# Optimization experiments

Measured on AMD Instinct MI355X. Metric: run time of the kernel, lower is better.

Reference implementation:

```python
import jax, jax.numpy as jnp
import numpy as np

N_BITS = 4            # W4A4 duquant-style fake quantization
BLOCK = 128           # rotation block size


def _round_ste(x):
    # straight-through rounding (matches round_ste used by LLM quantizers)
    return x + jax.lax.stop_gradient(jnp.round(x) - x)


def _block_rotate(x, R):
    # apply block-diagonal rotation along the last dim: x[..., F] -> x[..., F]
    *lead, F = x.shape
    B = R.shape[0]
    xr = jnp.einsum('...kb,bc->...kc', x.reshape(*lead, F // B, B), R)
    return xr.reshape(*lead, F)


def _fake_quant(x, R, n_bits):
    # rotate -> dynamic asymmetric uniform quant over last dim -> dequant -> de-rotate
    qmax = 2 ** n_bits - 1
    xr = _block_rotate(x, R)
    xmin = jnp.minimum(xr.min(axis=-1, keepdims=True), 0.0)
    xmax = jnp.maximum(xr.max(axis=-1, keepdims=True), 0.0)
    scale = jnp.clip((xmax - xmin) / qmax, 1e-5, None)
    zero_point = jax.lax.stop_gradient(jnp.round(-xmin / scale))
    xq = jnp.clip(_round_ste(xr / scale) + zero_point, 0.0, float(qmax))
    xdq = (xq - zero_point) * scale
    return _block_rotate(xdq, R.T)


def setup_inputs() -> dict:
    key = jax.random.key(0)
    k1, k2, k3 = jax.random.split(key, 3)
    x = jax.random.normal(k1, (4, 2048, 4096), dtype=jnp.float32)
    weight = jax.random.normal(k2, (4096, 4096), dtype=jnp.float32) * 0.02
    bias = jax.random.normal(k3, (4096,), dtype=jnp.float32) * 0.01
    # fixed orthogonal rotation matrix (DuQuant learned/constructed rotation)
    rng = np.random.default_rng(0)
    Rnp, _ = np.linalg.qr(rng.standard_normal((BLOCK, BLOCK)).astype(np.float32))
    R = jnp.asarray(Rnp, dtype=jnp.float32)
    return {"input": x, "weight": weight, "bias": bias, "R": R}


def reference(input, weight, bias, R):
    # act fake-quant (use_act_quant=True), weight fake-quant (use_weight_quant=True)
    x_q = _fake_quant(input, R, N_BITS)        # [B, S, Fin]
    w_q = _fake_quant(weight, R, N_BITS)       # [Fout, Fin], per-out-channel quant
    out = jnp.einsum('bsi,oi->bso', x_q, w_q) + bias
    return out
```

## Files before the change

kernel.cpp:

```cpp
#include <hip/hip_runtime.h>
#include <hip/hip_bf16.h>
#include <stdint.h>


typedef __bf16    bf16x8 __attribute__((ext_vector_type(8)));
typedef float     f32x4  __attribute__((ext_vector_type(4)));
typedef int       i32x4  __attribute__((ext_vector_type(4)));
typedef uint32_t  u32;
typedef uint32_t  u32x4  __attribute__((ext_vector_type(4)));

__device__ __forceinline__ void gload_lds16(const void* g, void* l) {
  __builtin_amdgcn_global_load_lds(
      (__attribute__((address_space(1))) void*)(g),
      (__attribute__((address_space(3))) void*)(l), 16, 0, 0);
}

__global__ __launch_bounds__(256)
void prep_rt(const float* __restrict__ R, unsigned short* __restrict__ RT3)
{
  const int tid = blockIdx.x * 256 + threadIdx.x;
  const int q  = tid & 7;
  const int l  = (tid >> 3) & 63;
  const int f  = (tid >> 9) & 7;
  const int ks = tid >> 12;
  const float v = R[(ks * 32 + (l >> 4) * 8 + q) * 128 + f * 16 + (l & 15)];
  __hip_bfloat16 h1 = __float2bfloat16(v);
  const float rem = v - __bfloat162float(h1);
  __hip_bfloat16 h2 = __float2bfloat16(rem);
  const float rem2 = rem - __bfloat162float(h2);
  __hip_bfloat16 h3 = __float2bfloat16(rem2);
  RT3[tid]          = *(unsigned short*)&h1;
  RT3[16384 + tid]  = *(unsigned short*)&h2;
  RT3[32768 + tid]  = *(unsigned short*)&h3;
}

#define FQ_TB  98304
#define FQ_SC  (98304 + 8 * 2560)

__global__ __launch_bounds__(512, 2)
void fq_rot1p(const float* __restrict__ X,
              const unsigned short* __restrict__ RT3,
              uint8_t* __restrict__ Q,
              float4* __restrict__ stats)
{
  __shared__ __align__(16) char lds[98304 + 8 * 2560 + 1664];

  const int t = threadIdx.x, lane = t & 63, wid = t >> 6;
  const size_t rowbase = (size_t)blockIdx.x * 16;
  const int colw = wid * 512;

#pragma unroll
  for (int i = 0; i < 12; ++i)
    gload_lds16((const char*)RT3 + i * 8192 + t * 16, lds + i * 8192 + t * 16);
  asm volatile("s_waitcnt vmcnt(0)" ::: "memory");
  __syncthreads();

  float* smin  = (float*)(lds + FQ_SC);
  float* smax  = (float*)(lds + FQ_SC + 512);
  float* rowsc = (float*)(lds + FQ_SC + 1024);
  float* rowzp = (float*)(lds + FQ_SC + 1088);
  int*   qsumL = (int*)  (lds + FQ_SC + 1152);

  const float* xbase = X + (rowbase + (lane & 15)) * 4096 + colw + (lane >> 4) * 8;

  f32x4 acc[4][8];
#pragma unroll
  for (int b = 0; b < 4; ++b)
#pragma unroll
    for (int f = 0; f < 8; ++f) acc[b][f] = (f32x4){0.f, 0.f, 0.f, 0.f};

#pragma unroll 1
  for (int kk = 0; kk < 4; ++kk) {
    union { bf16x8 v; unsigned short u[8]; } xh[4], xl[4], x2[4];
#pragma unroll
    for (int b = 0; b < 4; ++b) {
      const f32x4 lo = *(const f32x4*)(xbase + b * 128 + kk * 32);
      const f32x4 hi = *(const f32x4*)(xbase + b * 128 + kk * 32 + 4);
#pragma unroll
      for (int e = 0; e < 8; ++e) {
        const float xv = (e < 4) ? lo[e] : hi[e - 4];
        __hip_bfloat16 h1 = __float2bfloat16(xv);
        const float rm = xv - __bfloat162float(h1);
        __hip_bfloat16 h2 = __float2bfloat16(rm);
        const float rm2 = rm - __bfloat162float(h2);
        __hip_bfloat16 h3 = __float2bfloat16(rm2);
        xh[b].u[e] = *(unsigned short*)&h1;
        xl[b].u[e] = *(unsigned short*)&h2;
        x2[b].u[e] = *(unsigned short*)&h3;
      }
    }
#pragma unroll
    for (int f = 0; f < 8; ++f) {
      const int off = ((kk * 8 + f) * 64 + lane) * 16;
      const bf16x8 bh = *(const bf16x8*)(lds + off);
      const bf16x8 bl = *(const bf16x8*)(lds + 32768 + off);
      const bf16x8 b2 = *(const bf16x8*)(lds + 65536 + off);
#pragma unroll
      for (int b = 0; b < 4; ++b) {
        acc[b][f] = __builtin_amdgcn_mfma_f32_16x16x32_bf16(bh, xh[b].v, acc[b][f], 0, 0, 0);
        acc[b][f] = __builtin_amdgcn_mfma_f32_16x16x32_bf16(bh, xl[b].v, acc[b][f], 0, 0, 0);
        acc[b][f] = __builtin_amdgcn_mfma_f32_16x16x32_bf16(bh, x2[b].v, acc[b][f], 0, 0, 0);
        acc[b][f] = __builtin_amdgcn_mfma_f32_16x16x32_bf16(bl, xh[b].v, acc[b][f], 0, 0, 0);
        acc[b][f] = __builtin_amdgcn_mfma_f32_16x16x32_bf16(bl, xl[b].v, acc[b][f], 0, 0, 0);
        acc[b][f] = __builtin_amdgcn_mfma_f32_16x16x32_bf16(b2, xh[b].v, acc[b][f], 0, 0, 0);
      }
    }
  }

  float mn = 0.f, mx = 0.f;
#pragma unroll
  for (int b = 0; b < 4; ++b)
#pragma unroll
    for (int f = 0; f < 8; ++f)
#pragma unroll
      for (int r = 0; r < 4; ++r) {
        mn = fminf(mn, acc[b][f][r]);
        mx = fmaxf(mx, acc[b][f][r]);
      }
  mn = fminf(mn, __shfl_xor(mn, 16, 64));
  mn = fminf(mn, __shfl_xor(mn, 32, 64));
  mx = fmaxf(mx, __shfl_xor(mx, 16, 64));
  mx = fmaxf(mx, __shfl_xor(mx, 32, 64));
  if (lane < 16) { smin[wid * 16 + lane] = mn; smax[wid * 16 + lane] = mx; }
  __syncthreads();
  if (t < 16) {
    float m = 0.f, M = 0.f;
#pragma unroll
    for (int q = 0; q < 8; ++q) {
      m = fminf(m, smin[q * 16 + t]);
      M = fmaxf(M, smax[q * 16 + t]);
    }
    const float sc = fmaxf((M - m) / 15.0f, 1e-5f);
    rowsc[t] = sc;
    rowzp[t] = rintf(-m / sc);
  }
  __syncthreads();
  const float scale = rowsc[lane & 15];
  const float zp    = rowzp[lane & 15];

  u32* tw = (u32*)(lds + FQ_TB + wid * 2560);
  int qsum = 0;
#pragma unroll
  for (int b = 0; b < 4; ++b) {
#pragma unroll
    for (int f = 0; f < 8; ++f) {
      u32 pk = 0;
#pragma unroll
      for (int r = 0; r < 4; ++r) {
        const float qf = fminf(fmaxf(rintf(acc[b][f][r] / scale) + zp, 0.0f), 15.0f);
        const int qi = (int)qf;
        qsum += qi;
        pk |= (u32)qi << (8 * r);
      }
      tw[(lane & 15) * 40 + f * 4 + (lane >> 4)] = pk;
    }
#pragma unroll
    for (int rr = 0; rr < 2; ++rr) {
      const int row = rr * 8 + (lane >> 3);
      const int ch  = lane & 7;
      const u32x4 v = *(const u32x4*)&tw[row * 40 + ch * 4];
      *(u32x4*)(Q + (rowbase + row) * 4096 + colw + b * 128 + ch * 16) = v;
    }
  }

  qsum += __shfl_xor(qsum, 16, 64);
  qsum += __shfl_xor(qsum, 32, 64);
  if (lane < 16) qsumL[wid * 16 + lane] = qsum;
  __syncthreads();
  if (t < 16) {
    int S = 0;
#pragma unroll
    for (int q = 0; q < 8; ++q) S += qsumL[q * 16 + t];
    stats[rowbase + t] = make_float4(rowsc[t], rowzp[t], (float)S, 0.0f);
  }
}

__global__ __launch_bounds__(256)
void prep_cols(const float4* __restrict__ Wst, float* __restrict__ colS,
               float* __restrict__ colA, float* __restrict__ colB)
{
  const int n = blockIdx.x * 256 + threadIdx.x;
  const float4 w = Wst[n];
  colS[n] = w.x;
  colA[n] = w.x * w.z - 4096.0f * w.x * w.y;
  colB[n] = w.x * w.y;
}

#define NT 32

__global__ __launch_bounds__(512, 2)
void gemm256_8ph_i8(const uint8_t* __restrict__ Ap,
                    const uint8_t* __restrict__ Bp,
                    const float4* __restrict__ Xst,
                    const float* __restrict__ colS,
                    const float* __restrict__ colA,
                    const float* __restrict__ colB,
                    const float* __restrict__ bias,
                    float* __restrict__ C)
{
  __shared__ __align__(16) uint8_t lds[131072];
  char* ldsB = (char*)lds;
  const char* ldsc = (const char*)lds;

  const int tid  = threadIdx.x;
  const int lane = tid & 63;
  const int wid  = tid >> 6;
  const int wm   = wid >> 2;
  const int wn   = wid & 3;

  int bid = blockIdx.x;
  int nwg = gridDim.x;
  int swz = ((nwg & 7) == 0) ? ((bid & 7) * (nwg >> 3) + (bid >> 3)) : bid;
  const int bm = (swz >> 4) * 256;
  const int bn = (swz & 15) * 256;

  const int t16 = tid * 16;
  int stOff0, stOff1;
  {
    int Lb0 = t16;
    int Lb1 = t16 + 8192;
    int Lp0 = Lb0 ^ (((Lb0 >> 9) & 1) << 5);
    int Lp1 = Lb1 ^ (((Lb1 >> 9) & 1) << 5);
    int s0 = Lp0 >> 10, w0 = Lp0 & 1023;
    int s1 = Lp1 >> 10, w1 = Lp1 & 1023;
    int r0 = ((s0 >> 1) << 4) | (w0 >> 6);
    int k0 = ((s0 & 1) << 6) | (w0 & 63);
    int r1 = ((s1 >> 1) << 4) | (w1 >> 6);
    int k1 = ((s1 & 1) << 6) | (w1 & 63);
    stOff0 = r0 * 4096 + k0;
    stOff1 = r1 * 4096 + k1;
  }

  int swzw = (lane & 15) * 64 + (lane >> 4) * 16;
  swzw ^= ((swzw & 512) ? 32 : 0);

#define STAGE(GP, GROW, KT, SLOT) do {                                   \
    const uint8_t* _g = (GP) + ((size_t)(GROW)) * 4096 + (KT);           \
    gload_lds16(_g + stOff0, ldsB + (SLOT) + t16);                       \
    gload_lds16(_g + stOff1, ldsB + (SLOT) + 8192 + t16);                \
  } while (0)

  i32x4 acc[8][4];
#pragma unroll
  for (int i = 0; i < 8; ++i)
#pragma unroll
    for (int j = 0; j < 4; ++j) acc[i][j] = (i32x4){0, 0, 0, 0};

  STAGE(Bp, bn,       0, 32768);
  STAGE(Ap, bm,       0, 0);
  STAGE(Ap, bm + 128, 0, 16384);
  STAGE(Bp, bn + 128, 0, 49152);
  asm volatile("s_waitcnt vmcnt(4)" ::: "memory");
  STAGE(Bp, bn,       128, 65536 + 32768);
  STAGE(Ap, bm,       128, 65536);
  STAGE(Ap, bm + 128, 128, 65536 + 16384);
  asm volatile("s_waitcnt vmcnt(6)" ::: "memory");
  __builtin_amdgcn_s_barrier();

  const int wmOff = wm * 16384;
  const int wnOff = (wn >> 1) * 16384 + (wn & 1) * 8192;

#define LDA(P, I, KK) (*(const i32x4*)((P) + ((I) * 2 + (KK)) * 1024))
#define LDB(P, J, KK) (*(const i32x4*)((P) + ((J) * 2 + (KK)) * 1024))

#define MF8(I, AK0, AK1)                                                      \
  acc[I][0] = __builtin_amdgcn_mfma_i32_16x16x64_i8(AK0, b00, acc[I][0], 0, 0, 0); \
  acc[I][1] = __builtin_amdgcn_mfma_i32_16x16x64_i8(AK0, b10, acc[I][1], 0, 0, 0); \
  acc[I][2] = __builtin_amdgcn_mfma_i32_16x16x64_i8(AK0, b20, acc[I][2], 0, 0, 0); \
  acc[I][3] = __builtin_amdgcn_mfma_i32_16x16x64_i8(AK0, b30, acc[I][3], 0, 0, 0); \
  acc[I][0] = __builtin_amdgcn_mfma_i32_16x16x64_i8(AK1, b01, acc[I][0], 0, 0, 0); \
  acc[I][1] = __builtin_amdgcn_mfma_i32_16x16x64_i8(AK1, b11, acc[I][1], 0, 0, 0); \
  acc[I][2] = __builtin_amdgcn_mfma_i32_16x16x64_i8(AK1, b21, acc[I][2], 0, 0, 0); \
  acc[I][3] = __builtin_amdgcn_mfma_i32_16x16x64_i8(AK1, b31, acc[I][3], 0, 0, 0);

#define TILE(T, D) do {                                                       \
    const char* aP = ldsc + (D) * 65536 + wmOff + swzw;                       \
    const char* bP = ldsc + (D) * 65536 + 32768 + wnOff + swzw;               \
    i32x4 b00 = LDB(bP, 0, 0), b01 = LDB(bP, 0, 1);                           \
    i32x4 b10 = LDB(bP, 1, 0), b11 = LDB(bP, 1, 1);                           \
    i32x4 b20 = LDB(bP, 2, 0), b21 = LDB(bP, 2, 1);                           \
    i32x4 b30 = LDB(bP, 3, 0), b31 = LDB(bP, 3, 1);                           \
    i32x4 a00 = LDA(aP, 0, 0), a01 = LDA(aP, 0, 1);                           \
    i32x4 a10 = LDA(aP, 1, 0), a11 = LDA(aP, 1, 1);                           \
    if ((T) + 1 < NT) STAGE(Bp, bn + 128, ((T) + 1) * 128, ((D) ^ 1) * 65536 + 49152); \
    __builtin_amdgcn_s_barrier();                                             \
    asm volatile("s_waitcnt lgkmcnt(0)" ::: "memory");                        \
    __builtin_amdgcn_s_setprio(1);                                            \
    MF8(0, a00, a01); MF8(1, a10, a11);                                       \
    __builtin_amdgcn_s_setprio(0);                                            \
    __builtin_amdgcn_sched_barrier(0);                                        \
    __builtin_amdgcn_s_barrier();                                             \
    i32x4 a20 = LDA(aP, 2, 0), a21 = LDA(aP, 2, 1);                           \
    i32x4 a30 = LDA(aP, 3, 0), a31 = LDA(aP, 3, 1);                           \
    i32x4 a40 = LDA(aP, 4, 0), a41 = LDA(aP, 4, 1);                           \
    i32x4 a50 = LDA(aP, 5, 0), a51 = LDA(aP, 5, 1);                           \
    i32x4 a60 = LDA(aP, 6, 0), a61 = LDA(aP, 6, 1);                           \
    i32x4 a70 = LDA(aP, 7, 0), a71 = LDA(aP, 7, 1);                           \
    if ((T) + 2 < NT) STAGE(Bp, bn, ((T) + 2) * 128, (D) * 65536 + 32768);    \
    __builtin_amdgcn_s_barrier();                                             \
    asm volatile("s_waitcnt lgkmcnt(8)" ::: "memory");                        \
    __builtin_amdgcn_s_setprio(1);                                            \
    MF8(2, a20, a21); MF8(3, a30, a31);                                       \
    __builtin_amdgcn_s_setprio(0);                                            \
    __builtin_amdgcn_sched_barrier(0);                                        \
    __builtin_amdgcn_s_barrier();                                             \
    if ((T) + 2 < NT) STAGE(Ap, bm, ((T) + 2) * 128, (D) * 65536);            \
    __builtin_amdgcn_s_barrier();                                             \
    __builtin_amdgcn_s_setprio(1);                                            \
    MF8(4, a40, a41); MF8(5, a50, a51);                                       \
    __builtin_amdgcn_s_setprio(0);                                            \
    __builtin_amdgcn_sched_barrier(0);                                        \
    __builtin_amdgcn_s_barrier();                                             \
    if ((T) + 2 < NT) STAGE(Ap, bm + 128, ((T) + 2) * 128, (D) * 65536 + 16384); \
    __builtin_amdgcn_s_barrier();                                             \
    __builtin_amdgcn_s_setprio(1);                                            \
    MF8(6, a60, a61); MF8(7, a70, a71);                                       \
    __builtin_amdgcn_s_setprio(0);                                            \
    if ((T) + 2 < NT)      { asm volatile("s_waitcnt vmcnt(6)" ::: "memory"); } \
    else if ((T) + 1 < NT) { asm volatile("s_waitcnt vmcnt(0)" ::: "memory"); } \
    __builtin_amdgcn_sched_barrier(0);                                        \
    __builtin_amdgcn_s_barrier();                                             \
  } while (0)

  for (int t = 0; t < NT; t += 2) {
    TILE(t, 0);
    TILE(t + 1, 1);
  }

  {
    float* tile = (float*)ldsB;
    const int P = 268;
#pragma unroll 1
    for (int quarter = 0; quarter < 4; ++quarter) {
      __builtin_amdgcn_s_barrier();
      if (wm == (quarter >> 1)) {
        const int qi0 = (quarter & 1) * 4;
#pragma unroll
        for (int i = 0; i < 4; ++i)
#pragma unroll
          for (int j = 0; j < 4; ++j) {
            const int rl = i * 16 + (lane >> 4) * 4;
            const int cl = wn * 64 + j * 16 + (lane & 15);
#pragma unroll
            for (int r = 0; r < 4; ++r)
              tile[(rl + r) * P + cl] = (float)acc[qi0 + i][j][r];
          }
      }
      __builtin_amdgcn_s_barrier();
#pragma unroll 1
      for (int rr = 0; rr < 8; ++rr) {
        const int rl = wid * 8 + rr;
        const int grow = bm + quarter * 64 + rl;
        const float4 xs4 = Xst[grow];
        const float r1 = xs4.x, r2 = xs4.x * xs4.y, r3 = xs4.x * xs4.z;
        const int n0 = bn + lane * 4;
        const float4 v  = *(const float4*)&tile[rl * P + lane * 4];
        const float4 cs = *(const float4*)&colS[n0];
        const float4 ca = *(const float4*)&colA[n0];
        const float4 cb = *(const float4*)&colB[n0];
        const float4 bi = *(const float4*)&bias[n0];
        float4 o;
        o.x = r1 * cs.x * v.x - r2 * ca.x - r3 * cb.x + bi.x;
        o.y = r1 * cs.y * v.y - r2 * ca.y - r3 * cb.y + bi.y;
        o.z = r1 * cs.z * v.z - r2 * ca.z - r3 * cb.z + bi.z;
        o.w = r1 * cs.w * v.w - r2 * ca.w - r3 * cb.w + bi.w;
        *(float4*)&C[(size_t)grow * 4096 + n0] = o;
      }
    }
  }
#undef TILE
#undef MF8
#undef LDA
#undef LDB
#undef STAGE
}

extern "C" void kernel_launch(void* const* d_in, const int* in_sizes, int n_in,
                              void* d_out, int out_size, void* d_ws, size_t ws_size,
                              hipStream_t stream)
{
  const float* x    = (const float*)d_in[0];
  const float* wgt  = (const float*)d_in[1];
  const float* bias = (const float*)d_in[2];
  const float* R    = (const float*)d_in[3];

  const int K = 4096, N = 4096;
  const int M = in_sizes[0] / K;

  uint8_t* Qx = (uint8_t*)d_ws;
  uint8_t* Qw = Qx + (size_t)M * K;
  float4*  Sx = (float4*)(Qw + (size_t)N * K);
  float4*  Sw = Sx + M;
  unsigned short* RT3 = (unsigned short*)(Sw + N);
  float* colS = (float*)((char*)RT3 + 98304);
  float* colA = colS + N;
  float* colB = colA + N;

  prep_rt<<<64, 256, 0, stream>>>(R, RT3);
  fq_rot1p<<<M / 16, 512, 0, stream>>>(x,   RT3, Qx, Sx);
  fq_rot1p<<<N / 16, 512, 0, stream>>>(wgt, RT3, Qw, Sw);
  prep_cols<<<N / 256, 256, 0, stream>>>(Sw, colS, colA, colB);

  const int nblk = (M / 256) * (N / 256);
  gemm256_8ph_i8<<<nblk, 512, 0, stream>>>(Qx, Qw, Sx, colS, colA, colB, bias,
                                           (float*)d_out);
}
```

Before: 326.8 us.

## Replace pipelined 256x256 int8 GEMM with simple 128x128 tiled kernel

Swaps the 512-thread, double-buffered, phase-interleaved 256x256 int8 MFMA GEMM for a 256-thread 128x128 kernel with a single 16KB LDS buffer and two barriers per 64-wide K step. The epilogue writes dequantized results straight from registers instead of staging through LDS. This aims at higher occupancy and simpler code, but gives up data reuse, load/compute overlap and coalesced output stores.

```diff
diff --git a/kernel.cpp b/kernel.cpp
--- a/kernel.cpp
+++ b/kernel.cpp
@@ -186,193 +186,100 @@
   colB[n] = w.x * w.y;
 }
 
-#define NT 32
-
-__global__ __launch_bounds__(512, 2)
-void gemm256_8ph_i8(const uint8_t* __restrict__ Ap,
-                    const uint8_t* __restrict__ Bp,
-                    const float4* __restrict__ Xst,
-                    const float* __restrict__ colS,
-                    const float* __restrict__ colA,
-                    const float* __restrict__ colB,
-                    const float* __restrict__ bias,
-                    float* __restrict__ C)
-{
-  __shared__ __align__(16) uint8_t lds[131072];
+__global__ __launch_bounds__(256, 4)
+void gemm128_i8(const uint8_t* __restrict__ Ap,
+                const uint8_t* __restrict__ Bp,
+                const float4* __restrict__ Xst,
+                const float* __restrict__ colS,
+                const float* __restrict__ colA,
+                const float* __restrict__ colB,
+                const float* __restrict__ bias,
+                float* __restrict__ C)
+{
+  __shared__ __align__(16) uint8_t lds[16384];
   char* ldsB = (char*)lds;
   const char* ldsc = (const char*)lds;
 
   const int tid  = threadIdx.x;
   const int lane = tid & 63;
   const int wid  = tid >> 6;
-  const int wm   = wid >> 2;
-  const int wn   = wid & 3;
+  const int wm   = wid >> 1;
+  const int wn   = wid & 1;
 
   int bid = blockIdx.x;
   int nwg = gridDim.x;
   int swz = ((nwg & 7) == 0) ? ((bid & 7) * (nwg >> 3) + (bid >> 3)) : bid;
-  const int bm = (swz >> 4) * 256;
-  const int bn = (swz & 15) * 256;
+  const int bm = (swz >> 5) * 128;
+  const int bn = (swz & 31) * 128;
 
   const int t16 = tid * 16;
   int stOff0, stOff1;
   {
     int Lb0 = t16;
-    int Lb1 = t16 + 8192;
+    int Lb1 = t16 + 4096;
     int Lp0 = Lb0 ^ (((Lb0 >> 9) & 1) << 5);
     int Lp1 = Lb1 ^ (((Lb1 >> 9) & 1) << 5);
-    int s0 = Lp0 >> 10, w0 = Lp0 & 1023;
-    int s1 = Lp1 >> 10, w1 = Lp1 & 1023;
-    int r0 = ((s0 >> 1) << 4) | (w0 >> 6);
-    int k0 = ((s0 & 1) << 6) | (w0 & 63);
-    int r1 = ((s1 >> 1) << 4) | (w1 >> 6);
-    int k1 = ((s1 & 1) << 6) | (w1 & 63);
+    int r0 = ((Lp0 >> 10) << 4) | ((Lp0 & 1023) >> 6);
+    int k0 = Lp0 & 63;
+    int r1 = ((Lp1 >> 10) << 4) | ((Lp1 & 1023) >> 6);
+    int k1 = Lp1 & 63;
     stOff0 = r0 * 4096 + k0;
     stOff1 = r1 * 4096 + k1;
   }
 
-  int swzw = (lane & 15) * 64 + (lane >> 4) * 16;
-  swzw ^= ((swzw & 512) ? 32 : 0);
-
-#define STAGE(GP, GROW, KT, SLOT) do {                                   \
+  int swzr = (lane & 15) * 64 + (lane >> 4) * 16;
+  swzr ^= ((swzr & 512) ? 32 : 0);
+
+#define STG(GP, GROW, KT, SLOT) do {                                     \
     const uint8_t* _g = (GP) + ((size_t)(GROW)) * 4096 + (KT);           \
     gload_lds16(_g + stOff0, ldsB + (SLOT) + t16);                       \
-    gload_lds16(_g + stOff1, ldsB + (SLOT) + 8192 + t16);                \
+    gload_lds16(_g + stOff1, ldsB + (SLOT) + 4096 + t16);                \
   } while (0)
 
-  i32x4 acc[8][4];
-#pragma unroll
-  for (int i = 0; i < 8; ++i)
+  i32x4 acc[4][4];
+#pragma unroll
+  for (int i = 0; i < 4; ++i)
 #pragma unroll
     for (int j = 0; j < 4; ++j) acc[i][j] = (i32x4){0, 0, 0, 0};
 
-  STAGE(Bp, bn,       0, 32768);
-  STAGE(Ap, bm,       0, 0);
-  STAGE(Ap, bm + 128, 0, 16384);
-  STAGE(Bp, bn + 128, 0, 49152);
-  asm volatile("s_waitcnt vmcnt(4)" ::: "memory");
-  STAGE(Bp, bn,       128, 65536 + 32768);
-  STAGE(Ap, bm,       128, 65536);
-  STAGE(Ap, bm + 128, 128, 65536 + 16384);
-  asm volatile("s_waitcnt vmcnt(6)" ::: "memory");
-  __builtin_amdgcn_s_barrier();
-
-  const int wmOff = wm * 16384;
-  const int wnOff = (wn >> 1) * 16384 + (wn & 1) * 8192;
-
-#define LDA(P, I, KK) (*(const i32x4*)((P) + ((I) * 2 + (KK)) * 1024))
-#define LDB(P, J, KK) (*(const i32x4*)((P) + ((J) * 2 + (KK)) * 1024))
-
-#define MF8(I, AK0, AK1)                                                      \
-  acc[I][0] = __builtin_amdgcn_mfma_i32_16x16x64_i8(AK0, b00, acc[I][0], 0, 0, 0); \
-  acc[I][1] = __builtin_amdgcn_mfma_i32_16x16x64_i8(AK0, b10, acc[I][1], 0, 0, 0); \
-  acc[I][2] = __builtin_amdgcn_mfma_i32_16x16x64_i8(AK0, b20, acc[I][2], 0, 0, 0); \
-  acc[I][3] = __builtin_amdgcn_mfma_i32_16x16x64_i8(AK0, b30, acc[I][3], 0, 0, 0); \
-  acc[I][0] = __builtin_amdgcn_mfma_i32_16x16x64_i8(AK1, b01, acc[I][0], 0, 0, 0); \
-  acc[I][1] = __builtin_amdgcn_mfma_i32_16x16x64_i8(AK1, b11, acc[I][1], 0, 0, 0); \
-  acc[I][2] = __builtin_amdgcn_mfma_i32_16x16x64_i8(AK1, b21, acc[I][2], 0, 0, 0); \
-  acc[I][3] = __builtin_amdgcn_mfma_i32_16x16x64_i8(AK1, b31, acc[I][3], 0, 0, 0);
-
-#define TILE(T, D) do {                                                       \
-    const char* aP = ldsc + (D) * 65536 + wmOff + swzw;                       \
-    const char* bP = ldsc + (D) * 65536 + 32768 + wnOff + swzw;               \
-    i32x4 b00 = LDB(bP, 0, 0), b01 = LDB(bP, 0, 1);                           \
-    i32x4 b10 = LDB(bP, 1, 0), b11 = LDB(bP, 1, 1);                           \
-    i32x4 b20 = LDB(bP, 2, 0), b21 = LDB(bP, 2, 1);                           \
-    i32x4 b30 = LDB(bP, 3, 0), b31 = LDB(bP, 3, 1);                           \
-    i32x4 a00 = LDA(aP, 0, 0), a01 = LDA(aP, 0, 1);                           \
-    i32x4 a10 = LDA(aP, 1, 0), a11 = LDA(aP, 1, 1);                           \
-    if ((T) + 1 < NT) STAGE(Bp, bn + 128, ((T) + 1) * 128, ((D) ^ 1) * 65536 + 49152); \
-    __builtin_amdgcn_s_barrier();                                             \
-    asm volatile("s_waitcnt lgkmcnt(0)" ::: "memory");                        \
-    __builtin_amdgcn_s_setprio(1);                                            \
-    MF8(0, a00, a01); MF8(1, a10, a11);                                       \
-    __builtin_amdgcn_s_setprio(0);                                            \
-    __builtin_amdgcn_sched_barrier(0);                                        \
-    __builtin_amdgcn_s_barrier();                                             \
-    i32x4 a20 = LDA(aP, 2, 0), a21 = LDA(aP, 2, 1);                           \
-    i32x4 a30 = LDA(aP, 3, 0), a31 = LDA(aP, 3, 1);                           \
-    i32x4 a40 = LDA(aP, 4, 0), a41 = LDA(aP, 4, 1);                           \
-    i32x4 a50 = LDA(aP, 5, 0), a51 = LDA(aP, 5, 1);                           \
-    i32x4 a60 = LDA(aP, 6, 0), a61 = LDA(aP, 6, 1);                           \
-    i32x4 a70 = LDA(aP, 7, 0), a71 = LDA(aP, 7, 1);                           \
-    if ((T) + 2 < NT) STAGE(Bp, bn, ((T) + 2) * 128, (D) * 65536 + 32768);    \
-    __builtin_amdgcn_s_barrier();                                             \
-    asm volatile("s_waitcnt lgkmcnt(8)" ::: "memory");                        \
-    __builtin_amdgcn_s_setprio(1);                                            \
-    MF8(2, a20, a21); MF8(3, a30, a31);                                       \
-    __builtin_amdgcn_s_setprio(0);                                            \
-    __builtin_amdgcn_sched_barrier(0);                                        \
-    __builtin_amdgcn_s_barrier();                                             \
-    if ((T) + 2 < NT) STAGE(Ap, bm, ((T) + 2) * 128, (D) * 65536);            \
-    __builtin_amdgcn_s_barrier();                                             \
-    __builtin_amdgcn_s_setprio(1);                                            \
-    MF8(4, a40, a41); MF8(5, a50, a51);                                       \
-    __builtin_amdgcn_s_setprio(0);                                            \
-    __builtin_amdgcn_sched_barrier(0);                                        \
-    __builtin_amdgcn_s_barrier();                                             \
-    if ((T) + 2 < NT) STAGE(Ap, bm + 128, ((T) + 2) * 128, (D) * 65536 + 16384); \
-    __builtin_amdgcn_s_barrier();                                             \
-    __builtin_amdgcn_s_setprio(1);                                            \
-    MF8(6, a60, a61); MF8(7, a70, a71);                                       \
-    __builtin_amdgcn_s_setprio(0);                                            \
-    if ((T) + 2 < NT)      { asm volatile("s_waitcnt vmcnt(6)" ::: "memory"); } \
-    else if ((T) + 1 < NT) { asm volatile("s_waitcnt vmcnt(0)" ::: "memory"); } \
-    __builtin_amdgcn_sched_barrier(0);                                        \
-    __builtin_amdgcn_s_barrier();                                             \
-  } while (0)
-
-  for (int t = 0; t < NT; t += 2) {
-    TILE(t, 0);
-    TILE(t + 1, 1);
-  }
-
-  {
-    float* tile = (float*)ldsB;
-    const int P = 268;
-#pragma unroll 1
-    for (int quarter = 0; quarter < 4; ++quarter) {
-      __builtin_amdgcn_s_barrier();
-      if (wm == (quarter >> 1)) {
-        const int qi0 = (quarter & 1) * 4;
-#pragma unroll
-        for (int i = 0; i < 4; ++i)
-#pragma unroll
-          for (int j = 0; j < 4; ++j) {
-            const int rl = i * 16 + (lane >> 4) * 4;
-            const int cl = wn * 64 + j * 16 + (lane & 15);
-#pragma unroll
-            for (int r = 0; r < 4; ++r)
-              tile[(rl + r) * P + cl] = (float)acc[qi0 + i][j][r];
-          }
-      }
-      __builtin_amdgcn_s_barrier();
-#pragma unroll 1
-      for (int rr = 0; rr < 8; ++rr) {
-        const int rl = wid * 8 + rr;
-        const int grow = bm + quarter * 64 + rl;
-        const float4 xs4 = Xst[grow];
-        const float r1 = xs4.x, r2 = xs4.x * xs4.y, r3 = xs4.x * xs4.z;
-        const int n0 = bn + lane * 4;
-        const float4 v  = *(const float4*)&tile[rl * P + lane * 4];
-        const float4 cs = *(const float4*)&colS[n0];
-        const float4 ca = *(const float4*)&colA[n0];
-        const float4 cb = *(const float4*)&colB[n0];
-        const float4 bi = *(const float4*)&bias[n0];
-        float4 o;
-        o.x = r1 * cs.x * v.x - r2 * ca.x - r3 * cb.x + bi.x;
-        o.y = r1 * cs.y * v.y - r2 * ca.y - r3 * cb.y + bi.y;
-        o.z = r1 * cs.z * v.z - r2 * ca.z - r3 * cb.z + bi.z;
-        o.w = r1 * cs.w * v.w - r2 * ca.w - r3 * cb.w + bi.w;
-        *(float4*)&C[(size_t)grow * 4096 + n0] = o;
-      }
-    }
-  }
-#undef TILE
-#undef MF8
-#undef LDA
-#undef LDB
-#undef STAGE
+  for (int kt = 0; kt < 4096; kt += 64) {
+    __syncthreads();
+    STG(Ap, bm, kt, 0);
+    STG(Bp, bn, kt, 8192);
+    __syncthreads();
+
+    i32x4 fa[4], fb[4];
+#pragma unroll
+    for (int i = 0; i < 4; ++i)
+      fa[i] = *(const i32x4*)(ldsc + (wm * 4 + i) * 1024 + swzr);
+#pragma unroll
+    for (int j = 0; j < 4; ++j)
+      fb[j] = *(const i32x4*)(ldsc + 8192 + (wn * 4 + j) * 1024 + swzr);
+
+#pragma unroll
+    for (int i = 0; i < 4; ++i)
+#pragma unroll
+      for (int j = 0; j < 4; ++j)
+        acc[i][j] = __builtin_amdgcn_mfma_i32_16x16x64_i8(fa[i], fb[j], acc[i][j], 0, 0, 0);
+  }
+
+#pragma unroll
+  for (int j = 0; j < 4; ++j) {
+    const int n = bn + wn * 64 + j * 16 + (lane & 15);
+    const float cs = colS[n], ca = colA[n], cb = colB[n], bv = bias[n];
+#pragma unroll
+    for (int i = 0; i < 4; ++i) {
+      const int m0 = bm + wm * 64 + i * 16 + (lane >> 4) * 4;
+#pragma unroll
+      for (int r = 0; r < 4; ++r) {
+        const float4 xst = Xst[m0 + r];
+        const float d = (float)acc[i][j][r];
+        C[(size_t)(m0 + r) * 4096 + n] =
+            xst.x * cs * d - (xst.x * xst.y) * ca - (xst.x * xst.z) * cb + bv;
+      }
+    }
+  }
+#undef STG
 }
 
 extern "C" void kernel_launch(void* const* d_in, const int* in_sizes, int n_in,
@@ -401,7 +308,7 @@
   fq_rot1p<<<N / 16, 512, 0, stream>>>(wgt, RT3, Qw, Sw);
   prep_cols<<<N / 256, 256, 0, stream>>>(Sw, colS, colA, colB);
 
-  const int nblk = (M / 256) * (N / 256);
-  gemm256_8ph_i8<<<nblk, 512, 0, stream>>>(Qx, Qw, Sx, colS, colA, colB, bias,
-                                           (float*)d_out);
-}
+  const int nblk = (M / 128) * (N / 128);
+  gemm128_i8<<<nblk, 256, 0, stream>>>(Qx, Qw, Sx, colS, colA, colB, bias,
+                                       (float*)d_out);
+}
```

After: 363.5 us. 11.2% more time.
